# Kernel optimization log

Measured on AMD Instinct MI355X. Metric: run time of the kernel, lower is better.

Reference implementation:

```python
import jax, jax.numpy as jnp
import numpy as np

B, S, N, D, NAMED, NTYPES = 8, 64, 100, 1024, 768, 5

def _ln(x, g, b, eps=1e-5):
    m = x.mean(-1, keepdims=True)
    v = ((x - m) ** 2).mean(-1, keepdims=True)
    return (x - m) * jax.lax.rsqrt(v + eps) * g + b

def _lin(x, W, b=None):
    y = x @ W.T
    return y if b is None else y + b

def setup_inputs():
    key = jax.random.key(0)
    ks = jax.random.split(key, 24)
    p = lambda i, shape, s=0.02: jax.random.normal(ks[i], shape, jnp.float32) * s
    inp = {}
    inp['scene_reps'] = jax.random.normal(ks[0], (B, S, D), jnp.float32)
    u = jax.random.uniform(ks[1], (B, N, S))
    keep = (jax.random.uniform(ks[2], (B, N, S)) < 0.25).astype(jnp.float32)
    inp['incidence_matrix'] = u * keep
    inp['edge_type_ids'] = jax.random.randint(ks[3], (B, S), 0, NTYPES)
    inp['entity_type_ids'] = jax.random.randint(ks[4], (B, N), 0, NTYPES)
    inp['entity_mask'] = jax.random.uniform(ks[5], (B, N)) < 0.9
    inp['entity_name_embs'] = jax.random.normal(ks[6], (B, N, NAMED), jnp.float32)
    inp['type_embed'] = p(7, (NTYPES, D), 1.0)
    inp['name_W'] = p(8, (D, NAMED))
    inp['name_ln_g'] = jnp.ones(D); inp['name_ln_b'] = jnp.zeros(D)
    inp['n2e_W'] = p(9, (D, D)); inp['n2e_b'] = jnp.zeros(D)
    inp['t2e_W'] = p(10, (D, D)); inp['t2e_b'] = jnp.zeros(D)
    inp['edge_ln_g'] = jnp.ones(D); inp['edge_ln_b'] = jnp.zeros(D)
    inp['gate_W1'] = p(11, (D // 4, D)); inp['gate_b1'] = jnp.zeros(D // 4)
    inp['gate_W2'] = p(12, (3, D // 4)); inp['gate_b2'] = jnp.zeros(3)
    inp['ms_W'] = p(13, (D, D)); inp['ms_b'] = jnp.zeros(D)
    inp['ma_W'] = p(14, (D, D)); inp['ma_b'] = jnp.zeros(D)
    inp['mi_W'] = p(15, (D, D)); inp['mi_b'] = jnp.zeros(D)
    inp['role_w'] = p(16, (D,))
    inp['gru_Wih'] = p(17, (3 * D, D)); inp['gru_Whh'] = p(18, (3 * D, D))
    inp['gru_bih'] = jnp.zeros(3 * D); inp['gru_bhh'] = jnp.zeros(3 * D)
    inp['upd_ln_g'] = jnp.ones(D); inp['upd_ln_b'] = jnp.zeros(D)
    inp['eo_W'] = p(19, (D, D)); inp['eo_b'] = jnp.zeros(D)
    inp['eo_ln_g'] = jnp.ones(D); inp['eo_ln_b'] = jnp.zeros(D)
    inp['res_ln_g'] = jnp.ones(D); inp['res_ln_b'] = jnp.zeros(D)
    return inp

def reference(scene_reps, incidence_matrix, edge_type_ids, entity_type_ids, entity_mask, entity_name_embs, type_embed, name_W, name_ln_g, name_ln_b, n2e_W, n2e_b, t2e_W, t2e_b, edge_ln_g, edge_ln_b, gate_W1, gate_b1, gate_W2, gate_b2, ms_W, ms_b, ma_W, ma_b, mi_W, mi_b, role_w, gru_Wih, gru_Whh, gru_bih, gru_bhh, upd_ln_g, upd_ln_b, eo_W, eo_b, eo_ln_g, eo_ln_b, res_ln_g, res_ln_b):
    # edge_type_ids is accepted by the torch module but unused in its forward.
    dt = scene_reps.dtype
    emaskf = entity_mask.astype(dt)  # [B,N]
    h0 = type_embed[entity_type_ids] + _ln(_lin(entity_name_embs, name_W), name_ln_g, name_ln_b)
    h0 = h0 * emaskf[..., None]
    eye = jnp.eye(N, dtype=dt)
    step_ids = jnp.arange(S)

    def step(carry, xs):
        h, ebuf = carry  # h [B,N,D], ebuf [B,S,D] (hyperedge history)
        s, x_s, inc_s = xs  # x_s [B,D], inc_s [B,N]
        roles = inc_s * emaskf
        wsum = jnp.maximum(roles.sum(1, keepdims=True), 1.0)
        mean_ent = jnp.einsum('bn,bnd->bd', roles, h) / wsum
        e_s = _ln(_lin(mean_ent, n2e_W, n2e_b) + _lin(x_s, t2e_W, t2e_b), edge_ln_g, edge_ln_b)
        in_mask = (roles > 0).astype(dt)[..., None]  # [B,N,1]
        msg_scene = _lin(e_s, ms_W, ms_b)[:, None, :]
        # arc stream: attention over past hyperedges with exponential recency decay
        valid = (step_ids < s).astype(dt)
        denom = jnp.maximum(s - 1, 1).astype(dt)
        decay = jnp.exp(-1.0 + step_ids.astype(dt) / denom) * valid  # linspace(-1,0,s)
        arc = incidence_matrix * roles[:, :, None] * decay[None, None, :]  # [B,N,S]
        arc = arc / jnp.maximum(arc.sum(-1, keepdims=True), 1e-8)
        msg_arc = _lin(jnp.einsum('bns,bsd->bnd', arc, jax.lax.stop_gradient(ebuf)), ma_W, ma_b)
        msg_arc = jnp.where(s > 0, msg_arc, jnp.zeros_like(msg_arc))
        # interaction stream: entity co-occurrence within the scene
        co = roles[:, :, None] * roles[:, None, :] * (1.0 - eye)
        co = co / jnp.maximum(co.sum(-1, keepdims=True), 1e-8)
        msg_int = _lin(jnp.einsum('bnm,bmd->bnd', co, h), mi_W, mi_b)
        gate = jax.nn.softmax(_lin(jax.nn.gelu(_lin(e_s, gate_W1, gate_b1), approximate=False), gate_W2, gate_b2), axis=-1)  # [B,3]
        msg = gate[:, 0, None, None] * msg_scene + gate[:, 1, None, None] * msg_arc + gate[:, 2, None, None] * msg_int
        msg = msg + (roles[..., None] * role_w) * in_mask
        # GRUCell (torch semantics) + LayerNorm, masked update
        gi = _lin(msg, gru_Wih, gru_bih)
        gh = _lin(h, gru_Whh, gru_bhh)
        i_r, i_z, i_n = jnp.split(gi, 3, axis=-1)
        h_r, h_z, h_n = jnp.split(gh, 3, axis=-1)
        r = jax.nn.sigmoid(i_r + h_r)
        z = jax.nn.sigmoid(i_z + h_z)
        n = jnp.tanh(i_n + r * h_n)
        h_new = jnp.clip(_ln((1 - z) * n + z * h, upd_ln_g, upd_ln_b), -50.0, 50.0)
        h = h * (1 - in_mask) + h_new * in_mask
        ebuf = ebuf.at[:, s].set(e_s)
        return (h, ebuf), e_s

    ebuf0 = jnp.zeros((B, S, D), dt)
    (h_fin, _), es = jax.lax.scan(step, (h0, ebuf0), (step_ids, scene_reps.transpose(1, 0, 2), incidence_matrix.transpose(2, 0, 1)))
    H = es.transpose(1, 0, 2)  # [B,S,D]
    H = _ln(H + scene_reps, res_ln_g, res_ln_b)
    H = _ln(jax.nn.gelu(_lin(H, eo_W, eo_b), approximate=False), eo_ln_g, eo_ln_b)
    return (H, h_fin)
```

## Files before the change

### kernel.cpp

```cpp
#include <hip/hip_runtime.h>
#include <math.h>

#define B_   8
#define S_   64
#define N_   100
#define D_   1024
#define ND_  768
#define BN_  800
#define G3_  3072
#define G6_  6144
#define HC7  7168
#define RSC  0.00390625f

typedef _Float16 f16x8 __attribute__((ext_vector_type(8)));
typedef float f32x4 __attribute__((ext_vector_type(4)));

#define MFMA16(a,b,c) __builtin_amdgcn_mfma_f32_16x16x32_f16(a, b, c, 0, 0, 0)

static __device__ __forceinline__ float wave_sum(float v) {
    for (int off = 32; off > 0; off >>= 1) v += __shfl_down(v, off, 64);
    return v;
}

static __device__ __forceinline__ float block_sum(float v) {
    __shared__ float red_[8];
    float w = wave_sum(v);
    int lane = threadIdx.x & 63, wid = threadIdx.x >> 6;
    __syncthreads();
    if (lane == 0) red_[wid] = w;
    __syncthreads();
    float t = 0.f;
    for (int i = 0; i < 4; ++i) t += red_[i];
    return t;
}

static __device__ __forceinline__ float gelu_f(float x) {
    return 0.5f * x * (1.f + erff(x * 0.70710678118654752f));
}

static __device__ __forceinline__ unsigned short f2h(float x) {
    union { _Float16 h; unsigned short u; } c; c.h = (_Float16)x; return c.u;
}

__global__ __launch_bounds__(256) void k_f2h(
    const float* __restrict__ src, unsigned short* __restrict__ dst,
    int rows, int cols, int ldd)
{
    size_t n = (size_t)rows * cols;
    size_t i = ((size_t)blockIdx.x * 256 + threadIdx.x) * 4;
    if (i >= n) return;
    int r = (int)(i / cols);
    int c = (int)(i - (size_t)r * cols);
    float4 v = *(const float4*)(src + i);
    ushort4 o; o.x = f2h(v.x); o.y = f2h(v.y); o.z = f2h(v.z); o.w = f2h(v.w);
    *(ushort4*)(dst + (size_t)r * ldd + c) = o;
}

__global__ __launch_bounds__(256) void k_f2hT(
    const float* __restrict__ src, unsigned short* __restrict__ dst,
    int R, int C, int ldd, int rowoff)
{
    __shared__ _Float16 T[32][33];
    int tr = threadIdx.x >> 3, tc4 = (threadIdx.x & 7) * 4;
    int r0 = blockIdx.y * 32, c0 = blockIdx.x * 32;
    float4 v = *(const float4*)(src + (size_t)(r0 + tr) * C + c0 + tc4);
    T[tc4][tr] = (_Float16)v.x; T[tc4+1][tr] = (_Float16)v.y;
    T[tc4+2][tr] = (_Float16)v.z; T[tc4+3][tr] = (_Float16)v.w;
    __syncthreads();
    union { _Float16 h; unsigned short u; } cv;
    ushort4 o;
    cv.h = T[tr][tc4];   o.x = cv.u;
    cv.h = T[tr][tc4+1]; o.y = cv.u;
    cv.h = T[tr][tc4+2]; o.z = cv.u;
    cv.h = T[tr][tc4+3]; o.w = cv.u;
    *(ushort4*)(dst + (size_t)(rowoff + c0 + tr) * ldd + r0 + tc4) = o;
}

__global__ __launch_bounds__(256) void k_mfma16_nt(
    const unsigned short* __restrict__ A16, const unsigned short* __restrict__ W16,
    const float* __restrict__ bias, float* __restrict__ C,
    unsigned short* __restrict__ C16, float oscale,
    int M, int Nc, int K)
{
    int m0 = blockIdx.y * 64; if (m0 >= M) return;
    int n0 = blockIdx.x * 128;
    __shared__ _Float16 sA[64][72];
    __shared__ _Float16 sB[128][72];
    int tid = threadIdx.x;
    int w = tid >> 6, l = tid & 63;
    int l15 = l & 15, q = l >> 4;
    int wn = w * 32;
    int arow = tid >> 3, achk = (tid & 7) * 8;
    f32x4 acc[4][2] = {};
    for (int k0 = 0; k0 < K; k0 += 64) {
        for (int ri = 0; ri < 64; ri += 32) {
            int gm = m0 + arow + ri;
            uint4 v = make_uint4(0u, 0u, 0u, 0u);
            if (gm < M) v = *(const uint4*)(A16 + (size_t)gm * K + k0 + achk);
            *(uint4*)(&sA[arow + ri][achk]) = v;
        }
        for (int i = 0; i < 4; ++i) {
            int r = arow + 32 * i;
            *(uint4*)(&sB[r][achk]) = *(const uint4*)(W16 + (size_t)(n0 + r) * K + k0 + achk);
        }
        __syncthreads();
#pragma unroll
        for (int ks = 0; ks < 64; ks += 32) {
            f16x8 b0 = *(const f16x8*)(&sB[wn + l15][ks + q*8]);
            f16x8 b1 = *(const f16x8*)(&sB[wn + 16 + l15][ks + q*8]);
#pragma unroll
            for (int mi = 0; mi < 4; ++mi) {
                f16x8 a = *(const f16x8*)(&sA[mi*16 + l15][ks + q*8]);
                acc[mi][0] = MFMA16(a, b0, acc[mi][0]);
                acc[mi][1] = MFMA16(a, b1, acc[mi][1]);
            }
        }
        __syncthreads();
    }
    for (int mi = 0; mi < 4; ++mi)
        for (int nj = 0; nj < 2; ++nj)
            for (int r = 0; r < 4; ++r) {
                int gm = m0 + mi*16 + q*4 + r;
                int cl = wn + nj*16 + l15;
                if (gm < M) {
                    size_t off = (size_t)gm * Nc + n0 + cl;
                    float v = acc[mi][nj][r];
                    if (C16) C16[off] = f2h(v * oscale);
                    else C[off] = v + (bias ? bias[n0 + cl] : 0.f);
                }
            }
}

__global__ __launch_bounds__(256) void k_h0(
    const float* __restrict__ P, const int* __restrict__ etype,
    const int* __restrict__ emask, const float* __restrict__ temb,
    const float* __restrict__ g, const float* __restrict__ bt,
    float* __restrict__ h, unsigned short* __restrict__ h16)
{
    int bn = blockIdx.x, tid = threadIdx.x;
    int t = etype[bn], mk = emask[bn];
    float x[4]; float lsum = 0.f;
    for (int k = 0; k < 4; ++k) { x[k] = P[(size_t)bn*D_ + tid + 256*k]; lsum += x[k]; }
    float mean = block_sum(lsum) * (1.f / D_);
    float lv = 0.f;
    for (int k = 0; k < 4; ++k) { float d = x[k] - mean; lv += d * d; }
    float inv = rsqrtf(block_sum(lv) * (1.f / D_) + 1e-5f);
    for (int k = 0; k < 4; ++k) {
        int d = tid + 256*k;
        float y = (x[k] - mean) * inv * g[d] + bt[d];
        float hv = mk ? (temb[(size_t)t*D_ + d] + y) : 0.f;
        h[(size_t)bn*D_ + d] = hv;
        h16[(size_t)bn*D_ + d] = f2h(hv);
    }
}

__global__ __launch_bounds__(256) void k_hcat0(
    const unsigned short* __restrict__ h16, const unsigned short* __restrict__ n2e16,
    const unsigned short* __restrict__ Wmi16, const unsigned short* __restrict__ Whh16,
    float* __restrict__ Hcat)
{
    int m0 = blockIdx.y * 32;
    int n0 = blockIdx.x * 64;
    const unsigned short* Bp; int ldb; int nl;
    if (n0 < 1024)      { Bp = n2e16;        ldb = D_;  nl = n0; }
    else if (n0 < 4096) { Bp = Wmi16 + 2048; ldb = G3_; nl = n0 - 1024; }
    else                { Bp = Whh16;        ldb = D_;  nl = n0 - 4096; }
    __shared__ _Float16 sA[32][72];
    __shared__ _Float16 sB[64][72];
    int tid = threadIdx.x;
    int w = tid >> 6, l = tid & 63;
    int l15 = l & 15, q = l >> 4;
    int wm = (w & 1) * 16, wn = (w >> 1) * 32;
    int arow = tid >> 3, achk = (tid & 7) * 8;
    int gmA = m0 + arow;
    f32x4 acc[2] = {};
    for (int k0 = 0; k0 < D_; k0 += 64) {
        *(uint4*)(&sA[arow][achk]) = *(const uint4*)(h16 + (size_t)gmA*D_ + k0 + achk);
        *(uint4*)(&sB[arow][achk])      = *(const uint4*)(Bp + (size_t)(nl + arow)*ldb + k0 + achk);
        *(uint4*)(&sB[arow + 32][achk]) = *(const uint4*)(Bp + (size_t)(nl + arow + 32)*ldb + k0 + achk);
        __syncthreads();
#pragma unroll
        for (int ks = 0; ks < 64; ks += 32) {
            f16x8 a  = *(const f16x8*)(&sA[wm + l15][ks + q*8]);
            f16x8 b0 = *(const f16x8*)(&sB[wn + l15][ks + q*8]);
            f16x8 b1 = *(const f16x8*)(&sB[wn + 16 + l15][ks + q*8]);
            acc[0] = MFMA16(a, b0, acc[0]);
            acc[1] = MFMA16(a, b1, acc[1]);
        }
        __syncthreads();
    }
    for (int j = 0; j < 2; ++j)
        for (int r = 0; r < 4; ++r) {
            int row = wm + q*4 + r;
            Hcat[(size_t)(m0 + row)*HC7 + n0 + wn + j*16 + l15] = acc[j][r];
        }
}

__global__ __launch_bounds__(256) void k_front(
    const float* __restrict__ inc, const int* __restrict__ emask,
    const float* __restrict__ Esmi, float* __restrict__ arcsum,
    int* __restrict__ cntp, int* __restrict__ lst, float* __restrict__ rro,
    float* __restrict__ scl,
    const int* __restrict__ prevcnt, const int* __restrict__ prevlist,
    const unsigned short* __restrict__ h16, const unsigned short* __restrict__ n2e16,
    const unsigned short* __restrict__ Wmi16, const unsigned short* __restrict__ Whh16,
    float* __restrict__ Hcat, float* __restrict__ gatepre, int s)
{
    int tid = threadIdx.x, bid = blockIdx.x;
    if (bid == 0 && tid < 32) gatepre[tid] = 0.f;
    if (bid < BN_) {
        int m = bid;
        int b = m / N_;
        float r = emask[m] ? inc[(size_t)m*S_ + s] : 0.f;
        if (r <= 0.f) return;
        __shared__ int sidx, nwa;
        __shared__ float wav[S_]; __shared__ int wai[S_];
        if (tid == 0) { sidx = atomicAdd(cntp, 1); nwa = 0; }
        __syncthreads();
        int idx = sidx;
        float denomA = fmaxf((float)(s - 1), 1.f);
        float wa = 0.f;
        if (tid < s) {
            float iv = inc[(size_t)m*S_ + tid];
            if (iv > 0.f) {
                wa = iv * r * expf(-1.f + (float)tid / denomA);
                int p = atomicAdd(&nwa, 1);
                wav[p] = wa; wai[p] = tid;
            }
        }
        float dA = block_sum(wa);
        float rm = 0.f;
        if (tid < N_) rm = emask[b*N_ + tid] ? inc[((size_t)b*N_ + tid)*S_ + s] : 0.f;
        float wsum = block_sum(rm);
        __syncthreads();
        int na = nwa;
        float sclA = 1.f / fmaxf(dA, 1e-8f);
        if (tid == 0) {
            lst[idx] = m; rro[idx] = r;
            scl[idx] = r / fmaxf(r * (wsum - r), 1e-8f);
        }
        float a12[12];
#pragma unroll
        for (int k = 0; k < 12; ++k) a12[k] = 0.f;
        for (int j = 0; j < na; ++j) {
            float wj = wav[j];
            const float* ep = Esmi + ((size_t)b*S_ + wai[j])*G3_;
#pragma unroll
            for (int k = 0; k < 12; ++k) a12[k] += wj * ep[tid + 256*k];
        }
        float* ao = arcsum + (size_t)idx*G3_;
#pragma unroll
        for (int k = 0; k < 12; ++k) ao[tid + 256*k] = a12[k] * sclA;
    } else {
        int pM = *prevcnt;
        int t = bid - BN_;
        int nt = t % 112, mt = t / 112;
        int m0 = mt * 64;
        if (m0 >= pM) return;
        int n0 = nt * 64;
        const unsigned short* Bp; int ldb; int nl;
        if (n0 < 1024)      { Bp = n2e16;        ldb = D_;  nl = n0; }
        else if (n0 < 4096) { Bp = Wmi16 + 2048; ldb = G3_; nl = n0 - 1024; }
        else                { Bp = Whh16;        ldb = D_;  nl = n0 - 4096; }
        __shared__ _Float16 sA[64][72];
        __shared__ _Float16 sB[64][72];
        __shared__ int slist[64];
        if (tid < 64) {
            int gm = m0 + tid;
            slist[tid] = (gm < pM) ? prevlist[gm] : 0;
        }
        __syncthreads();
        int w = tid >> 6, l = tid & 63;
        int l15 = l & 15, q = l >> 4;
        int wm = (w & 1) * 32, wn = (w >> 1) * 32;
        int arow = tid >> 3, achk = (tid & 7) * 8;
        f32x4 acc[2][2] = {};
        for (int k0 = 0; k0 < D_; k0 += 64) {
            for (int ri = 0; ri < 64; ri += 32) {
                int row = arow + ri, gm = m0 + row;
                uint4 v = make_uint4(0u,0u,0u,0u);
                if (gm < pM) v = *(const uint4*)(h16 + (size_t)slist[row]*D_ + k0 + achk);
                *(uint4*)(&sA[row][achk]) = v;
            }
            *(uint4*)(&sB[arow][achk])      = *(const uint4*)(Bp + (size_t)(nl + arow)*ldb + k0 + achk);
            *(uint4*)(&sB[arow + 32][achk]) = *(const uint4*)(Bp + (size_t)(nl + arow + 32)*ldb + k0 + achk);
            __syncthreads();
#pragma unroll
            for (int ks = 0; ks < 64; ks += 32) {
                f16x8 a0 = *(const f16x8*)(&sA[wm + l15][ks + q*8]);
                f16x8 a1 = *(const f16x8*)(&sA[wm + 16 + l15][ks + q*8]);
                f16x8 b0 = *(const f16x8*)(&sB[wn + l15][ks + q*8]);
                f16x8 b1 = *(const f16x8*)(&sB[wn + 16 + l15][ks + q*8]);
                acc[0][0] = MFMA16(a0, b0, acc[0][0]);
                acc[0][1] = MFMA16(a0, b1, acc[0][1]);
                acc[1][0] = MFMA16(a1, b0, acc[1][0]);
                acc[1][1] = MFMA16(a1, b1, acc[1][1]);
            }
            __syncthreads();
        }
        for (int mi = 0; mi < 2; ++mi)
            for (int nj = 0; nj < 2; ++nj)
                for (int r = 0; r < 4; ++r) {
                    int row = wm + mi*16 + q*4 + r;
                    int gm = m0 + row;
                    if (gm < pM)
                        Hcat[(size_t)slist[row]*HC7 + n0 + wn + nj*16 + l15] = acc[mi][nj][r];
                }
    }
}

static __device__ void compute_es(
    int b, int s,
    const float* __restrict__ inc, const int* __restrict__ emask,
    const float* __restrict__ Hcat, const float* __restrict__ n2eb,
    const float* __restrict__ pre_t2e,
    const float* __restrict__ elng, const float* __restrict__ elnb,
    float* se)
{
    __shared__ float sw_[N_]; __shared__ int sidx_[N_]; __shared__ int snact_;
    int tid = threadIdx.x;
    if (tid == 0) snact_ = 0;
    __syncthreads();
    float r = 0.f;
    if (tid < N_) {
        r = emask[b*N_ + tid] ? inc[((size_t)b*N_ + tid)*S_ + s] : 0.f;
        if (r > 0.f) {
            int p = atomicAdd(&snact_, 1);
            sw_[p] = r; sidx_[p] = tid;
        }
    }
    float wsum = block_sum(r);
    int nact = snact_;
    float invw = 1.f / fmaxf(wsum, 1.f);
    float4 e = make_float4(0.f,0.f,0.f,0.f);
    for (int j = 0; j < nact; ++j) {
        float wj = sw_[j];
        float4 v = *((const float4*)(Hcat + (size_t)(b*N_ + sidx_[j])*HC7) + tid);
        e.x += wj*v.x; e.y += wj*v.y; e.z += wj*v.z; e.w += wj*v.w;
    }
    float4 nb = *((const float4*)n2eb + tid);
    float4 pt = *((const float4*)(pre_t2e + ((size_t)b*S_ + s)*D_) + tid);
    float x[4];
    x[0] = e.x*invw + nb.x + pt.x; x[1] = e.y*invw + nb.y + pt.y;
    x[2] = e.z*invw + nb.z + pt.z; x[3] = e.w*invw + nb.w + pt.w;
    float lsum = x[0] + x[1] + x[2] + x[3];
    float mean = block_sum(lsum) * (1.f / D_);
    float lv = 0.f;
    for (int k = 0; k < 4; ++k) { float d = x[k] - mean; lv += d * d; }
    float inv = rsqrtf(block_sum(lv) * (1.f / D_) + 1e-5f);
    float4 lg = *((const float4*)elng + tid);
    float4 lb = *((const float4*)elnb + tid);
    int d4 = tid * 4;
    se[d4]   = (x[0]-mean)*inv*lg.x + lb.x;
    se[d4+1] = (x[1]-mean)*inv*lg.y + lb.y;
    se[d4+2] = (x[2]-mean)*inv*lg.z + lb.z;
    se[d4+3] = (x[3]-mean)*inv*lg.w + lb.w;
    __syncthreads();
}

__global__ __launch_bounds__(256) void k_mid(
    const float* __restrict__ inc, const int* __restrict__ emask,
    const float* __restrict__ Hcat, const float* __restrict__ n2eb,
    const float* __restrict__ pre_t2e,
    const float* __restrict__ elng, const float* __restrict__ elnb,
    const float* __restrict__ gW1, const float* __restrict__ gb1,
    const float* __restrict__ gW2, const unsigned short* __restrict__ Wmi16,
    float* __restrict__ esbuf, float* __restrict__ gatepre,
    float* __restrict__ Tmi, float* __restrict__ Emi, float* __restrict__ Esmi,
    int* __restrict__ ctrl, int par, int s)
{
    int bid = blockIdx.x, tid = threadIdx.x;
    __shared__ float se[D_];
    if (bid < 32) {
        int b = bid >> 2, seg = bid & 3;
        if (bid == 0 && tid == 0) ctrl[1 - par] = 0;
        compute_es(b, s, inc, emask, Hcat, n2eb, pre_t2e, elng, elnb, se);
        if (seg == 0) {
            for (int k = 0; k < 4; ++k) {
                int d = tid + 256*k;
                esbuf[((size_t)b*S_ + s)*D_ + d] = se[d];
            }
        }
        if (tid < 64) {
            int u = seg * 64 + tid;
            float acc = gb1[u];
            const float* w1 = gW1 + (size_t)u * D_;
            for (int j = 0; j < D_; j += 4) {
                float4 w = *(const float4*)(w1 + j);
                acc += w.x*se[j] + w.y*se[j+1] + w.z*se[j+2] + w.w*se[j+3];
            }
            float hg = gelu_f(acc);
            for (int c = 0; c < 3; ++c) {
                float p = wave_sum(gW2[c*256 + u] * hg);
                if (tid == 0) atomicAdd(gatepre + b*4 + c, p);
            }
        }
    } else if (bid < 128) {
        int t = bid - 32;
        int b = t / 12, ch = t - b*12;
        __shared__ float sw_[N_]; __shared__ int sidx_[N_]; __shared__ int snact_;
        if (tid == 0) snact_ = 0;
        __syncthreads();
        if (tid < N_) {
            float r = emask[b*N_ + tid] ? inc[((size_t)b*N_ + tid)*S_ + s] : 0.f;
            if (r > 0.f) {
                int p = atomicAdd(&snact_, 1);
                sw_[p] = r; sidx_[p] = tid;
            }
        }
        __syncthreads();
        int nact = snact_;
        int col = ch * 256 + tid;
        float acc = 0.f;
        for (int j = 0; j < nact; ++j)
            acc += sw_[j] * Hcat[(size_t)(b*N_ + sidx_[j])*HC7 + 1024 + col];
        Tmi[(size_t)b*G3_ + col] = acc;
    } else {
        int t = bid - 128;
        int b = t / 48, u = t - b*48;
        int n0 = u * 64;
        compute_es(b, s, inc, emask, Hcat, n2eb, pre_t2e, elng, elnb, se);
        int coll = tid >> 2, kq = (tid & 3) * 256;
        int col = n0 + coll;
#pragma unroll
        for (int seg = 0; seg < 2; ++seg) {
            const unsigned short* pr = Wmi16 + (size_t)col * G3_ + seg*1024 + kq;
            float acc = 0.f;
            for (int kk = 0; kk < 256; kk += 8) {
                uint4 pv = *(const uint4*)(pr + kk);
                union { uint4 uu; _Float16 h[8]; } cv; cv.uu = pv;
#pragma unroll
                for (int j = 0; j < 8; ++j) acc += (float)cv.h[j] * se[kq + kk + j];
            }
            acc += __shfl_xor(acc, 1, 64);
            acc += __shfl_xor(acc, 2, 64);
            if ((tid & 3) == 0) {
                if (seg == 0) Emi[(size_t)b*G3_ + col] = acc;
                else Esmi[((size_t)b*S_ + s)*G3_ + col] = acc;
            }
        }
    }
}

__global__ __launch_bounds__(256) void k_fin(
    const int* __restrict__ lst, const int* __restrict__ cntp,
    const float* __restrict__ rro, const float* __restrict__ scl,
    const float* __restrict__ gatepre, const float* __restrict__ gb2,
    const float* __restrict__ Hcat, const float* __restrict__ Emi,
    const float* __restrict__ arcsum, const float* __restrict__ Tmi,
    const float* __restrict__ gBm, const float* __restrict__ bih,
    const float* __restrict__ bhh,
    const float* __restrict__ ulng, const float* __restrict__ ulnb,
    float* __restrict__ h, unsigned short* __restrict__ h16, int s)
{
    int row = blockIdx.x;
    if (row >= *cntp) return;
    int bn = lst[row];
    int b = bn / N_;
    int tid = threadIdx.x;
    float t0 = gatepre[b*4+0] + gb2[0];
    float t1 = gatepre[b*4+1] + gb2[1];
    float t2 = gatepre[b*4+2] + gb2[2];
    float mx = fmaxf(t0, fmaxf(t1, t2));
    float e0 = expf(t0-mx), e1 = expf(t1-mx), e2 = expf(t2-mx);
    float si = 1.f / (e0 + e1 + e2);
    float g0 = e0*si, g1 = (s > 0) ? e1*si : 0.f, g2 = e2*si;
    float rv = rro[row];
    float sI = scl[row];
    const float* Hrow = Hcat + (size_t)bn * HC7;
    const float* em = Emi + (size_t)b * G3_;
    const float* as = arcsum + (size_t)row * G3_;
    const float* tm = Tmi + (size_t)b * G3_;
    float u[4]; float lsum = 0.f;
    for (int k = 0; k < 4; ++k) {
        int d = tid + 256*k;
        float ip[3];
#pragma unroll
        for (int c = 0; c < 3; ++c) {
            int dd = c*D_ + d;
            float gint = tm[dd] - rv * Hrow[1024 + dd];
            ip[c] = RSC * (g0*em[dd] + g1*as[dd] + g2*sI*gint)
                  + g0*gBm[dd] + g1*gBm[G3_ + dd] + g2*gBm[2*G3_ + dd]
                  + rv*gBm[3*G3_ + dd] + bih[dd];
        }
        float hr = Hrow[4096 + d]        + bhh[d];
        float hz = Hrow[4096 + D_ + d]   + bhh[D_ + d];
        float hn = Hrow[4096 + 2*D_ + d] + bhh[2*D_ + d];
        float hv = h[(size_t)bn*D_ + d];
        float r = 1.f / (1.f + expf(-(ip[0] + hr)));
        float z = 1.f / (1.f + expf(-(ip[1] + hz)));
        float nn = tanhf(ip[2] + r * hn);
        u[k] = (1.f - z) * nn + z * hv;
        lsum += u[k];
    }
    float mean = block_sum(lsum) * (1.f / D_);
    float lv = 0.f;
    for (int k = 0; k < 4; ++k) { float d = u[k] - mean; lv += d * d; }
    float inv = rsqrtf(block_sum(lv) * (1.f / D_) + 1e-5f);
    for (int k = 0; k < 4; ++k) {
        int d = tid + 256*k;
        float y = (u[k] - mean) * inv * ulng[d] + ulnb[d];
        y = fminf(fmaxf(y, -50.f), 50.f);
        h[(size_t)bn*D_ + d] = y;
        h16[(size_t)bn*D_ + d] = f2h(y);
    }
}

__global__ __launch_bounds__(256) void k_resln(
    float* __restrict__ buf, const float* __restrict__ scene,
    const float* __restrict__ g, const float* __restrict__ bt,
    unsigned short* __restrict__ H16)
{
    size_t row = blockIdx.x;
    int tid = threadIdx.x;
    float x[4]; float lsum = 0.f;
    for (int k = 0; k < 4; ++k) {
        int d = tid + 256*k;
        x[k] = buf[row*D_ + d] + scene[row*D_ + d];
        lsum += x[k];
    }
    float mean = block_sum(lsum) * (1.f / D_);
    float lv = 0.f;
    for (int k = 0; k < 4; ++k) { float d = x[k] - mean; lv += d * d; }
    float inv = rsqrtf(block_sum(lv) * (1.f / D_) + 1e-5f);
    for (int k = 0; k < 4; ++k) {
        int d = tid + 256*k;
        float y = (x[k] - mean) * inv * g[d] + bt[d];
        buf[row*D_ + d] = y;
        H16[row*D_ + d] = f2h(y);
    }
}

__global__ __launch_bounds__(256) void k_final(
    const float* __restrict__ G, const float* __restrict__ g, const float* __restrict__ bt,
    float* __restrict__ outH, const float* __restrict__ h, float* __restrict__ outh)
{
    int tid = threadIdx.x;
    if (blockIdx.x < B_*S_) {
        size_t row = blockIdx.x;
        float x[4]; float lsum = 0.f;
        for (int k = 0; k < 4; ++k) {
            x[k] = gelu_f(G[row*D_ + tid + 256*k]);
            lsum += x[k];
        }
        float mean = block_sum(lsum) * (1.f / D_);
        float lv = 0.f;
        for (int k = 0; k < 4; ++k) { float d = x[k] - mean; lv += d * d; }
        float inv = rsqrtf(block_sum(lv) * (1.f / D_) + 1e-5f);
        for (int k = 0; k < 4; ++k) {
            int d = tid + 256*k;
            outH[row*D_ + d] = (x[k] - mean) * inv * g[d] + bt[d];
        }
    } else {
        size_t bn = blockIdx.x - B_*S_;
        for (int d = tid; d < D_; d += 256)
            outh[bn*D_ + d] = h[bn*D_ + d];
    }
}

extern "C" void kernel_launch(void* const* d_in, const int* in_sizes, int n_in,
                              void* d_out, int out_size, void* d_ws, size_t ws_size,
                              hipStream_t stream)
{
    const float* scene = (const float*)d_in[0];
    const float* inc   = (const float*)d_in[1];
    const int*   etype = (const int*)d_in[3];
    const int*   emask = (const int*)d_in[4];
    const float* nemb  = (const float*)d_in[5];
    const float* temb  = (const float*)d_in[6];
    const float* nameW = (const float*)d_in[7];
    const float* nlg   = (const float*)d_in[8];
    const float* nlb   = (const float*)d_in[9];
    const float* n2eW  = (const float*)d_in[10];
    const float* n2eb  = (const float*)d_in[11];
    const float* t2eW  = (const float*)d_in[12];
    const float* t2eb  = (const float*)d_in[13];
    const float* elng  = (const float*)d_in[14];
    const float* elnb  = (const float*)d_in[15];
    const float* gW1   = (const float*)d_in[16];
    const float* gb1   = (const float*)d_in[17];
    const float* gW2   = (const float*)d_in[18];
    const float* gb2   = (const float*)d_in[19];
    const float* msW   = (const float*)d_in[20];
    const float* msB   = (const float*)d_in[21];
    const float* maW   = (const float*)d_in[22];
    const float* maB   = (const float*)d_in[23];
    const float* miW   = (const float*)d_in[24];
    const float* miB   = (const float*)d_in[25];
    const float* rolew = (const float*)d_in[26];
    const float* Wih   = (const float*)d_in[27];
    const float* Whh   = (const float*)d_in[28];
    const float* bih   = (const float*)d_in[29];
    const float* bhh   = (const float*)d_in[30];
    const float* ulng  = (const float*)d_in[31];
    const float* ulnb  = (const float*)d_in[32];
    const float* eoW   = (const float*)d_in[33];
    const float* eoB   = (const float*)d_in[34];
    const float* eolng = (const float*)d_in[35];
    const float* eolnb = (const float*)d_in[36];
    const float* rlng  = (const float*)d_in[37];
    const float* rlnb  = (const float*)d_in[38];

    float* outH = (float*)d_out;
    float* outh = outH + (size_t)B_*S_*D_;

    float* W = (float*)d_ws;
    size_t o = 0;
    int*   ctrl     = (int*)(W + o); o += 64;
    float* gatepre  = W + o; o += 32;
    float* rowrole  = W + o; o += 2*BN_;
    float* sclbuf   = W + o; o += BN_;
    int*   list     = (int*)(W + o); o += 2*BN_;
    float* hbuf     = W + o; o += (size_t)BN_*D_;
    float* Hcat     = W + o; o += (size_t)BN_*HC7;
    float* pre_t2e  = W + o; o += (size_t)B_*S_*D_;
    float* gBm      = W + o; o += 4*G3_;
    float* Emi      = W + o; o += (size_t)B_*G3_;
    float* Esmi     = W + o; o += (size_t)B_*S_*G3_;
    float* arcsum   = W + o; o += (size_t)BN_*G3_;
    float* Tmi      = W + o; o += (size_t)B_*G3_;
    float* tmp      = W + o; o += (size_t)BN_*D_;
    unsigned short* U = (unsigned short*)(W + o);
    size_t uo = 0;
    unsigned short* h16    = U + uo; uo += (size_t)BN_*D_;
    unsigned short* H16    = U + uo; uo += (size_t)B_*S_*D_;
    unsigned short* Wih16  = U + uo; uo += (size_t)G3_*D_;
    unsigned short* Whh16  = U + uo; uo += (size_t)G3_*D_;
    unsigned short* n2e16  = U + uo; uo += (size_t)D_*D_;
    unsigned short* eoW16  = U + uo; uo += (size_t)D_*D_;
    unsigned short* nW16   = U + uo; uo += (size_t)D_*ND_;
    unsigned short* nE16   = U + uo; uo += (size_t)BN_*ND_;
    unsigned short* t2e16  = U + uo; uo += (size_t)D_*D_;
    unsigned short* sc16   = U + uo; uo += (size_t)B_*S_*D_;
    unsigned short* WcatT16= U + uo; uo += (size_t)G3_*D_;
    unsigned short* Wmi16  = U + uo; uo += (size_t)G3_*G3_;
    unsigned short* bias4  = U + uo; uo += 4*D_;

    hipMemsetAsync(ctrl, 0, 16, stream);

    #define CVT(src, dst, r, c, ld) \
        k_f2h<<<(((size_t)(r)*(c)/4 + 255)/256), 256, 0, stream>>>(src, dst, r, c, ld)
    CVT(Wih,   Wih16, G3_, D_,  D_);
    CVT(Whh,   Whh16, G3_, D_,  D_);
    CVT(n2eW,  n2e16, D_,  D_,  D_);
    CVT(nameW, nW16,  D_,  ND_, ND_);
    CVT(nemb,  nE16,  BN_, ND_, ND_);
    CVT(eoW,   eoW16, D_,  D_,  D_);
    CVT(t2eW,  t2e16, D_,  D_,  D_);
    CVT(scene, sc16,  B_*S_, D_, D_);
    CVT(msB,   bias4 + 0,    1, D_, D_);
    CVT(maB,   bias4 + D_,   1, D_, D_);
    CVT(miB,   bias4 + 2*D_, 1, D_, D_);
    CVT(rolew, bias4 + 3*D_, 1, D_, D_);
    #undef CVT
    k_f2hT<<<dim3(32,32), 256, 0, stream>>>(msW, WcatT16, D_, D_, D_, 0);
    k_f2hT<<<dim3(32,32), 256, 0, stream>>>(maW, WcatT16, D_, D_, D_, D_);
    k_f2hT<<<dim3(32,32), 256, 0, stream>>>(miW, WcatT16, D_, D_, D_, 2*D_);

    k_mfma16_nt<<<dim3(G3_/128, G3_/64), 256, 0, stream>>>(
        Wih16, WcatT16, nullptr, nullptr, Wmi16, 256.f, G3_, G3_, D_);
    k_mfma16_nt<<<dim3(G3_/128, 1), 256, 0, stream>>>(
        bias4, Wih16, nullptr, gBm, nullptr, 1.f, 4, G3_, D_);
    k_mfma16_nt<<<dim3(D_/128, (B_*S_+63)/64), 256, 0, stream>>>(
        sc16, t2e16, t2eb, pre_t2e, nullptr, 1.f, B_*S_, D_, D_);
    k_mfma16_nt<<<dim3(D_/128, (BN_+63)/64), 256, 0, stream>>>(
        nE16, nW16, nullptr, tmp, nullptr, 1.f, BN_, D_, ND_);
    k_h0<<<BN_, 256, 0, stream>>>(tmp, etype, emask, temb, nlg, nlb, hbuf, h16);
    k_hcat0<<<dim3(112, 25), 256, 0, stream>>>(h16, n2e16, Wmi16, Whh16, Hcat);

    for (int s = 0; s < S_; ++s) {
        int par = s & 1;
        int*   cntp = ctrl + par;
        int*   pcnt = ctrl + (1 - par);
        int*   lst  = list + par * BN_;
        int*   plst = list + (1 - par) * BN_;
        float* rro  = rowrole + par * BN_;
        k_front<<<BN_ + 112*13, 256, 0, stream>>>(inc, emask, Esmi, arcsum,
            cntp, lst, rro, sclbuf, pcnt, plst, h16, n2e16, Wmi16, Whh16,
            Hcat, gatepre, s);
        k_mid<<<512, 256, 0, stream>>>(inc, emask, Hcat, n2eb, pre_t2e,
            elng, elnb, gW1, gb1, gW2, Wmi16, outH, gatepre, Tmi, Emi, Esmi,
            ctrl, par, s);
        k_fin<<<BN_, 256, 0, stream>>>(lst, cntp, rro, sclbuf, gatepre, gb2,
            Hcat, Emi, arcsum, Tmi, gBm, bih, bhh, ulng, ulnb, hbuf, h16, s);
    }

    k_resln<<<B_*S_, 256, 0, stream>>>(outH, scene, rlng, rlnb, H16);
    k_mfma16_nt<<<dim3(D_/128, (B_*S_+63)/64), 256, 0, stream>>>(
        H16, eoW16, eoB, tmp, nullptr, 1.f, B_*S_, D_, D_);
    k_final<<<B_*S_ + BN_, 256, 0, stream>>>(tmp, eolng, eolnb, outH, hbuf, outh);
}
```

Baseline: 4.162 ms.

## Accumulate per-batch entity sums via atomics in k_front and batch the Wmi matvec

The per-batch weighted sums of Hcat (esum and Tmi) are now built inside k_front with atomicAdd. Rows updated in the previous step contribute from the GEMM epilogue, and unchanged rows contribute from the cached Hcat. k_mid therefore no longer rescans the active entities; it reads the accumulated sums from double-buffered arrays and zeroes the buffers for the next step. The Emi/Esmi matvec is restructured so that 96 blocks each handle 32 columns across all 8 batches, with each row of Wmi read once instead of once per batch, and the grid shrinks from 512 to 128 blocks. The cost is a large number of float atomics, nondeterministic summation order, and tricky correctness around which rows contribute at which step.

```diff
diff --git a/kernel.cpp b/kernel.cpp
--- a/kernel.cpp
+++ b/kernel.cpp
@@ -19,6 +19,11 @@
 
 static __device__ __forceinline__ float wave_sum(float v) {
     for (int off = 32; off > 0; off >>= 1) v += __shfl_down(v, off, 64);
+    return v;
+}
+
+static __device__ __forceinline__ float wave_allsum(float v) {
+    for (int off = 1; off < 64; off <<= 1) v += __shfl_xor(v, off, 64);
     return v;
 }
 
@@ -204,7 +209,9 @@
     const int* __restrict__ prevcnt, const int* __restrict__ prevlist,
     const unsigned short* __restrict__ h16, const unsigned short* __restrict__ n2e16,
     const unsigned short* __restrict__ Wmi16, const unsigned short* __restrict__ Whh16,
-    float* __restrict__ Hcat, float* __restrict__ gatepre, int s)
+    float* __restrict__ Hcat, float* __restrict__ gatepre,
+    float* __restrict__ esumP, float* __restrict__ TmiP, float* __restrict__ wsumP,
+    int s)
 {
     int tid = threadIdx.x, bid = blockIdx.x;
     if (bid == 0 && tid < 32) gatepre[tid] = 0.f;
@@ -238,6 +245,20 @@
         if (tid == 0) {
             lst[idx] = m; rro[idx] = r;
             scl[idx] = r / fmaxf(r * (wsum - r), 1e-8f);
+            wsumP[b] = wsum;
+        }
+        float rprev = (s > 0) ? inc[(size_t)m*S_ + (s-1)] : 0.f;
+        if (rprev <= 0.f) {
+            const float4* hp = (const float4*)(Hcat + (size_t)m*HC7);
+#pragma unroll
+            for (int j2 = 0; j2 < 4; ++j2) {
+                float4 hv = hp[tid + 256*j2];
+                int c = (tid + 256*j2) * 4;
+                float* dst = (c < 1024) ? (esumP + (size_t)b*D_ + c)
+                                        : (TmiP + (size_t)b*G3_ + (c - 1024));
+                atomicAdd(dst + 0, r*hv.x); atomicAdd(dst + 1, r*hv.y);
+                atomicAdd(dst + 2, r*hv.z); atomicAdd(dst + 3, r*hv.w);
+            }
         }
         float a12[12];
 #pragma unroll
@@ -265,9 +286,16 @@
         __shared__ _Float16 sA[64][72];
         __shared__ _Float16 sB[64][72];
         __shared__ int slist[64];
+        __shared__ float srn[64];
+        __shared__ int sbb[64];
         if (tid < 64) {
             int gm = m0 + tid;
-            slist[tid] = (gm < pM) ? prevlist[gm] : 0;
+            int m = (gm < pM) ? prevlist[gm] : 0;
+            slist[tid] = m;
+            float rn = 0.f;
+            if (gm < pM) rn = emask[m] ? inc[(size_t)m*S_ + s] : 0.f;
+            srn[tid] = rn;
+            sbb[tid] = m / N_;
         }
         __syncthreads();
         int w = tid >> 6, l = tid & 63;
@@ -303,84 +331,64 @@
                 for (int r = 0; r < 4; ++r) {
                     int row = wm + mi*16 + q*4 + r;
                     int gm = m0 + row;
-                    if (gm < pM)
-                        Hcat[(size_t)slist[row]*HC7 + n0 + wn + nj*16 + l15] = acc[mi][nj][r];
+                    if (gm < pM) {
+                        float v = acc[mi][nj][r];
+                        int c = n0 + wn + nj*16 + l15;
+                        Hcat[(size_t)slist[row]*HC7 + c] = v;
+                        float rn = srn[row];
+                        if (rn > 0.f && c < 4096) {
+                            float* dst = (c < 1024)
+                                ? (esumP + (size_t)sbb[row]*D_ + c)
+                                : (TmiP + (size_t)sbb[row]*G3_ + (c - 1024));
+                            atomicAdd(dst, rn * v);
+                        }
+                    }
                 }
     }
 }
 
-static __device__ void compute_es(
-    int b, int s,
-    const float* __restrict__ inc, const int* __restrict__ emask,
-    const float* __restrict__ Hcat, const float* __restrict__ n2eb,
-    const float* __restrict__ pre_t2e,
-    const float* __restrict__ elng, const float* __restrict__ elnb,
-    float* se)
-{
-    __shared__ float sw_[N_]; __shared__ int sidx_[N_]; __shared__ int snact_;
-    int tid = threadIdx.x;
-    if (tid == 0) snact_ = 0;
-    __syncthreads();
-    float r = 0.f;
-    if (tid < N_) {
-        r = emask[b*N_ + tid] ? inc[((size_t)b*N_ + tid)*S_ + s] : 0.f;
-        if (r > 0.f) {
-            int p = atomicAdd(&snact_, 1);
-            sw_[p] = r; sidx_[p] = tid;
-        }
-    }
-    float wsum = block_sum(r);
-    int nact = snact_;
-    float invw = 1.f / fmaxf(wsum, 1.f);
-    float4 e = make_float4(0.f,0.f,0.f,0.f);
-    for (int j = 0; j < nact; ++j) {
-        float wj = sw_[j];
-        float4 v = *((const float4*)(Hcat + (size_t)(b*N_ + sidx_[j])*HC7) + tid);
-        e.x += wj*v.x; e.y += wj*v.y; e.z += wj*v.z; e.w += wj*v.w;
-    }
-    float4 nb = *((const float4*)n2eb + tid);
-    float4 pt = *((const float4*)(pre_t2e + ((size_t)b*S_ + s)*D_) + tid);
-    float x[4];
-    x[0] = e.x*invw + nb.x + pt.x; x[1] = e.y*invw + nb.y + pt.y;
-    x[2] = e.z*invw + nb.z + pt.z; x[3] = e.w*invw + nb.w + pt.w;
-    float lsum = x[0] + x[1] + x[2] + x[3];
-    float mean = block_sum(lsum) * (1.f / D_);
-    float lv = 0.f;
-    for (int k = 0; k < 4; ++k) { float d = x[k] - mean; lv += d * d; }
-    float inv = rsqrtf(block_sum(lv) * (1.f / D_) + 1e-5f);
-    float4 lg = *((const float4*)elng + tid);
-    float4 lb = *((const float4*)elnb + tid);
-    int d4 = tid * 4;
-    se[d4]   = (x[0]-mean)*inv*lg.x + lb.x;
-    se[d4+1] = (x[1]-mean)*inv*lg.y + lb.y;
-    se[d4+2] = (x[2]-mean)*inv*lg.z + lb.z;
-    se[d4+3] = (x[3]-mean)*inv*lg.w + lb.w;
-    __syncthreads();
-}
-
 __global__ __launch_bounds__(256) void k_mid(
-    const float* __restrict__ inc, const int* __restrict__ emask,
-    const float* __restrict__ Hcat, const float* __restrict__ n2eb,
-    const float* __restrict__ pre_t2e,
+    const float* __restrict__ esumP, const float* __restrict__ wsumP,
+    float* __restrict__ esumZ, float* __restrict__ TmiZ, float* __restrict__ wsumZ,
+    const float* __restrict__ n2eb, const float* __restrict__ pre_t2e,
     const float* __restrict__ elng, const float* __restrict__ elnb,
     const float* __restrict__ gW1, const float* __restrict__ gb1,
     const float* __restrict__ gW2, const unsigned short* __restrict__ Wmi16,
     float* __restrict__ esbuf, float* __restrict__ gatepre,
-    float* __restrict__ Tmi, float* __restrict__ Emi, float* __restrict__ Esmi,
+    float* __restrict__ Emi, float* __restrict__ Esmi,
     int* __restrict__ ctrl, int par, int s)
 {
     int bid = blockIdx.x, tid = threadIdx.x;
-    __shared__ float se[D_];
     if (bid < 32) {
+        __shared__ float se[D_];
         int b = bid >> 2, seg = bid & 3;
         if (bid == 0 && tid == 0) ctrl[1 - par] = 0;
-        compute_es(b, s, inc, emask, Hcat, n2eb, pre_t2e, elng, elnb, se);
-        if (seg == 0) {
-            for (int k = 0; k < 4; ++k) {
-                int d = tid + 256*k;
-                esbuf[((size_t)b*S_ + s)*D_ + d] = se[d];
-            }
-        }
+        esumZ[(size_t)b*D_ + seg*256 + tid] = 0.f;
+#pragma unroll
+        for (int j = 0; j < 3; ++j) TmiZ[(size_t)b*G3_ + seg*768 + j*256 + tid] = 0.f;
+        if (seg == 0 && tid == 0) wsumZ[b] = 0.f;
+        float invw = 1.f / fmaxf(wsumP[b], 1.f);
+        float4 ev = ((const float4*)(esumP + (size_t)b*D_))[tid];
+        float4 nb = ((const float4*)n2eb)[tid];
+        float4 pt = ((const float4*)(pre_t2e + ((size_t)b*S_ + s)*D_))[tid];
+        float x[4] = { ev.x*invw + nb.x + pt.x, ev.y*invw + nb.y + pt.y,
+                       ev.z*invw + nb.z + pt.z, ev.w*invw + nb.w + pt.w };
+        float mean = block_sum(x[0]+x[1]+x[2]+x[3]) * (1.f / D_);
+        float lv = 0.f;
+#pragma unroll
+        for (int k = 0; k < 4; ++k) { float d = x[k] - mean; lv += d * d; }
+        float inv = rsqrtf(block_sum(lv) * (1.f / D_) + 1e-5f);
+        float4 lg = ((const float4*)elng)[tid];
+        float4 lb = ((const float4*)elnb)[tid];
+        float y0 = (x[0]-mean)*inv*lg.x + lb.x;
+        float y1 = (x[1]-mean)*inv*lg.y + lb.y;
+        float y2 = (x[2]-mean)*inv*lg.z + lb.z;
+        float y3 = (x[3]-mean)*inv*lg.w + lb.w;
+        int d4 = tid * 4;
+        se[d4] = y0; se[d4+1] = y1; se[d4+2] = y2; se[d4+3] = y3;
+        if (seg == 0)
+            ((float4*)(esbuf + ((size_t)b*S_ + s)*D_))[tid] = make_float4(y0,y1,y2,y3);
+        __syncthreads();
         if (tid < 64) {
             int u = seg * 64 + tid;
             float acc = gb1[u];
@@ -395,48 +403,107 @@
                 if (tid == 0) atomicAdd(gatepre + b*4 + c, p);
             }
         }
-    } else if (bid < 128) {
-        int t = bid - 32;
-        int b = t / 12, ch = t - b*12;
-        __shared__ float sw_[N_]; __shared__ int sidx_[N_]; __shared__ int snact_;
-        if (tid == 0) snact_ = 0;
-        __syncthreads();
-        if (tid < N_) {
-            float r = emask[b*N_ + tid] ? inc[((size_t)b*N_ + tid)*S_ + s] : 0.f;
-            if (r > 0.f) {
-                int p = atomicAdd(&snact_, 1);
-                sw_[p] = r; sidx_[p] = tid;
-            }
-        }
-        __syncthreads();
-        int nact = snact_;
-        int col = ch * 256 + tid;
-        float acc = 0.f;
-        for (int j = 0; j < nact; ++j)
-            acc += sw_[j] * Hcat[(size_t)(b*N_ + sidx_[j])*HC7 + 1024 + col];
-        Tmi[(size_t)b*G3_ + col] = acc;
     } else {
-        int t = bid - 128;
-        int b = t / 48, u = t - b*48;
-        int n0 = u * 64;
-        compute_es(b, s, inc, emask, Hcat, n2eb, pre_t2e, elng, elnb, se);
-        int coll = tid >> 2, kq = (tid & 3) * 256;
-        int col = n0 + coll;
-#pragma unroll
-        for (int seg = 0; seg < 2; ++seg) {
-            const unsigned short* pr = Wmi16 + (size_t)col * G3_ + seg*1024 + kq;
-            float acc = 0.f;
-            for (int kk = 0; kk < 256; kk += 8) {
-                uint4 pv = *(const uint4*)(pr + kk);
-                union { uint4 uu; _Float16 h[8]; } cv; cv.uu = pv;
-#pragma unroll
-                for (int j = 0; j < 8; ++j) acc += (float)cv.h[j] * se[kq + kk + j];
-            }
-            acc += __shfl_xor(acc, 1, 64);
-            acc += __shfl_xor(acc, 2, 64);
-            if ((tid & 3) == 0) {
-                if (seg == 0) Emi[(size_t)b*G3_ + col] = acc;
-                else Esmi[((size_t)b*S_ + s)*G3_ + col] = acc;
+        __shared__ float se32[8][1028];
+        int w = tid >> 6, lane = tid & 63;
+        for (int bb = 0; bb < 2; ++bb) {
+            int b = w*2 + bb;
+            float invw = 1.f / fmaxf(wsumP[b], 1.f);
+            int d0 = lane * 16;
+            const float4* ep = (const float4*)(esumP + (size_t)b*D_ + d0);
+            const float4* np = (const float4*)(n2eb + d0);
+            const float4* pp = (const float4*)(pre_t2e + ((size_t)b*S_ + s)*D_ + d0);
+            float x[16]; float sm = 0.f;
+#pragma unroll
+            for (int j = 0; j < 4; ++j) {
+                float4 e = ep[j], n = np[j], p = pp[j];
+                x[j*4+0] = e.x*invw + n.x + p.x;
+                x[j*4+1] = e.y*invw + n.y + p.y;
+                x[j*4+2] = e.z*invw + n.z + p.z;
+                x[j*4+3] = e.w*invw + n.w + p.w;
+                sm += x[j*4+0] + x[j*4+1] + x[j*4+2] + x[j*4+3];
+            }
+            float mean = wave_allsum(sm) * (1.f / D_);
+            float lv = 0.f;
+#pragma unroll
+            for (int j = 0; j < 16; ++j) { float d = x[j] - mean; lv += d * d; }
+            float inv = rsqrtf(wave_allsum(lv) * (1.f / D_) + 1e-5f);
+            const float4* lgp = (const float4*)(elng + d0);
+            const float4* lbp = (const float4*)(elnb + d0);
+#pragma unroll
+            for (int j = 0; j < 4; ++j) {
+                float4 lg = lgp[j], lb = lbp[j];
+                se32[b][d0 + j*4 + 0] = (x[j*4+0]-mean)*inv*lg.x + lb.x;
+                se32[b][d0 + j*4 + 1] = (x[j*4+1]-mean)*inv*lg.y + lb.y;
+                se32[b][d0 + j*4 + 2] = (x[j*4+2]-mean)*inv*lg.z + lb.z;
+                se32[b][d0 + j*4 + 3] = (x[j*4+3]-mean)*inv*lg.w + lb.w;
+            }
+        }
+        __syncthreads();
+        int c0 = (bid - 32) * 32;
+        int colg = tid >> 5, t31 = tid & 31;
+        int cb = c0 + colg * 4;
+        float accA[4][8] = {};
+        float accB[4][8] = {};
+#pragma unroll
+        for (int i = 0; i < 8; ++i) {
+            int kh = t31*4 + i*128;
+            float wf[4][4];
+#pragma unroll
+            for (int c = 0; c < 4; ++c) {
+                union { uint2 u; _Float16 h[4]; } cv;
+                cv.u = *(const uint2*)(Wmi16 + (size_t)(cb + c)*G3_ + kh);
+                wf[c][0] = (float)cv.h[0]; wf[c][1] = (float)cv.h[1];
+                wf[c][2] = (float)cv.h[2]; wf[c][3] = (float)cv.h[3];
+            }
+#pragma unroll
+            for (int b = 0; b < 8; ++b) {
+                float4 sv = *(const float4*)(&se32[b][kh]);
+#pragma unroll
+                for (int c = 0; c < 4; ++c)
+                    accA[c][b] += wf[c][0]*sv.x + wf[c][1]*sv.y
+                                + wf[c][2]*sv.z + wf[c][3]*sv.w;
+            }
+        }
+#pragma unroll
+        for (int i = 0; i < 8; ++i) {
+            int kh = t31*4 + i*128;
+            float wf[4][4];
+#pragma unroll
+            for (int c = 0; c < 4; ++c) {
+                union { uint2 u; _Float16 h[4]; } cv;
+                cv.u = *(const uint2*)(Wmi16 + (size_t)(cb + c)*G3_ + 1024 + kh);
+                wf[c][0] = (float)cv.h[0]; wf[c][1] = (float)cv.h[1];
+                wf[c][2] = (float)cv.h[2]; wf[c][3] = (float)cv.h[3];
+            }
+#pragma unroll
+            for (int b = 0; b < 8; ++b) {
+                float4 sv = *(const float4*)(&se32[b][kh]);
+#pragma unroll
+                for (int c = 0; c < 4; ++c)
+                    accB[c][b] += wf[c][0]*sv.x + wf[c][1]*sv.y
+                                + wf[c][2]*sv.z + wf[c][3]*sv.w;
+            }
+        }
+#pragma unroll
+        for (int off = 16; off >= 1; off >>= 1) {
+#pragma unroll
+            for (int c = 0; c < 4; ++c)
+#pragma unroll
+                for (int b = 0; b < 8; ++b) {
+                    accA[c][b] += __shfl_down(accA[c][b], off, 32);
+                    accB[c][b] += __shfl_down(accB[c][b], off, 32);
+                }
+        }
+        if (t31 == 0) {
+#pragma unroll
+            for (int c = 0; c < 4; ++c) {
+                int col = cb + c;
+#pragma unroll
+                for (int b = 0; b < 8; ++b) {
+                    Emi[(size_t)b*G3_ + col] = accA[c][b];
+                    Esmi[((size_t)b*S_ + s)*G3_ + col] = accB[c][b];
+                }
             }
         }
     }
@@ -607,6 +674,9 @@
     float* W = (float*)d_ws;
     size_t o = 0;
     int*   ctrl     = (int*)(W + o); o += 64;
+    float* esum2    = W + o; o += 2*(size_t)B_*D_;
+    float* Tmi2     = W + o; o += 2*(size_t)B_*G3_;
+    float* wsum2    = W + o; o += 16;
     float* gatepre  = W + o; o += 32;
     float* rowrole  = W + o; o += 2*BN_;
     float* sclbuf   = W + o; o += BN_;
@@ -618,7 +688,6 @@
     float* Emi      = W + o; o += (size_t)B_*G3_;
     float* Esmi     = W + o; o += (size_t)B_*S_*G3_;
     float* arcsum   = W + o; o += (size_t)BN_*G3_;
-    float* Tmi      = W + o; o += (size_t)B_*G3_;
     float* tmp      = W + o; o += (size_t)BN_*D_;
     unsigned short* U = (unsigned short*)(W + o);
     size_t uo = 0;
@@ -636,7 +705,8 @@
     unsigned short* Wmi16  = U + uo; uo += (size_t)G3_*G3_;
     unsigned short* bias4  = U + uo; uo += 4*D_;
 
-    hipMemsetAsync(ctrl, 0, 16, stream);
+    hipMemsetAsync(ctrl, 0,
+        (64 + 2*(size_t)B_*D_ + 2*(size_t)B_*G3_ + 16) * sizeof(float), stream);
 
     #define CVT(src, dst, r, c, ld) \
         k_f2h<<<(((size_t)(r)*(c)/4 + 255)/256), 256, 0, stream>>>(src, dst, r, c, ld)
@@ -675,14 +745,20 @@
         int*   lst  = list + par * BN_;
         int*   plst = list + (1 - par) * BN_;
         float* rro  = rowrole + par * BN_;
+        float* esumP = esum2 + (size_t)par * B_*D_;
+        float* esumZ = esum2 + (size_t)(1 - par) * B_*D_;
+        float* TmiP  = Tmi2 + (size_t)par * B_*G3_;
+        float* TmiZ  = Tmi2 + (size_t)(1 - par) * B_*G3_;
+        float* wsumP = wsum2 + par * 8;
+        float* wsumZ = wsum2 + (1 - par) * 8;
         k_front<<<BN_ + 112*13, 256, 0, stream>>>(inc, emask, Esmi, arcsum,
             cntp, lst, rro, sclbuf, pcnt, plst, h16, n2e16, Wmi16, Whh16,
-            Hcat, gatepre, s);
-        k_mid<<<512, 256, 0, stream>>>(inc, emask, Hcat, n2eb, pre_t2e,
-            elng, elnb, gW1, gb1, gW2, Wmi16, outH, gatepre, Tmi, Emi, Esmi,
-            ctrl, par, s);
+            Hcat, gatepre, esumP, TmiP, wsumP, s);
+        k_mid<<<128, 256, 0, stream>>>(esumP, wsumP, esumZ, TmiZ, wsumZ,
+            n2eb, pre_t2e, elng, elnb, gW1, gb1, gW2, Wmi16,
+            outH, gatepre, Emi, Esmi, ctrl, par, s);
         k_fin<<<BN_, 256, 0, stream>>>(lst, cntp, rro, sclbuf, gatepre, gb2,
-            Hcat, Emi, arcsum, Tmi, gBm, bih, bhh, ulng, ulnb, hbuf, h16, s);
+            Hcat, Emi, arcsum, TmiP, gBm, bih, bhh, ulng, ulnb, hbuf, h16, s);
     }
 
     k_resln<<<B_*S_, 256, 0, stream>>>(outH, scene, rlng, rlnb, H16);
```

Measured after the change: 4.203 ms. Within noise of the previous version (+1.0%).
